# Kernel tuning notes

Measured on AMD Instinct MI355X. Metric: run time of the kernel, lower is better.

## Reference

```python
import jax, jax.numpy as jnp
import numpy as np

EPS = 1e-12  # torch F.normalize default eps


def setup_inputs() -> dict:
    key = jax.random.key(0)
    k1, k2, k3 = jax.random.split(key, 3)
    B, T, S = 128, 512, 256
    emission_trajectory = jax.random.uniform(k1, (B, T, S), dtype=jnp.float32)
    weight = jax.random.normal(k2, (S, S), dtype=jnp.float32)
    initial_state = jax.random.normal(k3, (S,), dtype=jnp.float32)
    return {
        "emission_trajectory": emission_trajectory,
        "weight": weight,
        "initial_state": initial_state,
    }


def reference(emission_trajectory, weight, initial_state):
    B, T, S = emission_trajectory.shape
    # row-stochastic transition matrix (softmax over dim=1)
    transition = jax.nn.softmax(weight, axis=1)  # [S, S]
    # initial belief (training path: softmax of learned logits), broadcast to batch
    next_state0 = jnp.broadcast_to(jax.nn.softmax(initial_state), (B, S))

    emissions_t = jnp.swapaxes(emission_trajectory, 0, 1)  # [T, B, S]

    def step(next_state, emission_k):
        # Bayes update: elementwise likelihood, L1 normalize (torch p=1 normalize)
        unnorm = next_state * emission_k  # [B, S]
        l1 = jnp.sum(jnp.abs(unnorm), axis=1, keepdims=True)
        state = unnorm / jnp.maximum(l1, EPS)
        # predict: small GEMM [B,S] @ [S,S]
        next_state = state @ transition
        return next_state, next_state

    _, traj = jax.lax.scan(step, next_state0, emissions_t)  # traj: [T, B, S]
    return jnp.swapaxes(traj, 0, 1)  # [B, T, S]
```

## Files before the change

kernel.cpp:

```cpp
#include <hip/hip_runtime.h>
#include <stdint.h>

namespace {

constexpr int Tn = 512;
constexpr int Sn = 256;
constexpr float EPS = 1e-12f;

typedef _Float16 f16x8 __attribute__((ext_vector_type(8)));
typedef float    f32x4 __attribute__((ext_vector_type(4)));

__device__ __forceinline__ void wg_barrier_lds() {
    asm volatile("s_waitcnt lgkmcnt(0)" ::: "memory");
    __builtin_amdgcn_s_barrier();
}

__launch_bounds__(256, 1)
__global__ void hmm_kernel(const float* __restrict__ emission,
                           const float* __restrict__ weight,
                           const float* __restrict__ init,
                           float* __restrict__ out)
{
    const int tid  = threadIdx.x;
    const int wv   = tid >> 6;
    const int lane = tid & 63;
    const int g    = lane >> 4;
    const int jj   = lane & 15;
    const int b    = blockIdx.x;

    __shared__ __align__(16) _Float16 wf16[2][Sn];
    __shared__ __align__(16) float    s_m[Sn];
    __shared__ __align__(16) float    s_z[Sn];

    {
        const float* wr = weight + (size_t)tid * Sn;
        float m = -3.402823466e38f;
        #pragma unroll 4
        for (int i = 0; i < Sn; i += 4) {
            float4 v = *reinterpret_cast<const float4*>(wr + i);
            m = fmaxf(m, fmaxf(fmaxf(v.x, v.y), fmaxf(v.z, v.w)));
        }
        float z0 = 0.f, z1 = 0.f, z2 = 0.f, z3 = 0.f;
        #pragma unroll 4
        for (int i = 0; i < Sn; i += 4) {
            float4 v = *reinterpret_cast<const float4*>(wr + i);
            z0 += expf(v.x - m); z1 += expf(v.y - m);
            z2 += expf(v.z - m); z3 += expf(v.w - m);
        }
        s_m[tid] = m;
        s_z[tid] = 1.f / ((z0 + z1) + (z2 + z3));
        __syncthreads();
    }

    f16x8 bf[4][8];
    #pragma unroll
    for (int s = 0; s < 4; ++s) {
        const int col = 64 * wv + 16 * s + jj;
        #pragma unroll
        for (int ck = 0; ck < 8; ++ck) {
            #pragma unroll
            for (int i = 0; i < 8; ++i) {
                const int k = ck * 32 + g * 8 + i;
                bf[s][ck][i] =
                    (_Float16)(expf(weight[(size_t)k * Sn + col] - s_m[k]) * s_z[k]);
            }
        }
    }
    const f16x8 ones8 = {(_Float16)1.f, (_Float16)1.f, (_Float16)1.f, (_Float16)1.f,
                         (_Float16)1.f, (_Float16)1.f, (_Float16)1.f, (_Float16)1.f};

    const float* em = emission + (size_t)b * Tn * Sn + tid;
    float*       op = out      + (size_t)b * Tn * Sn + tid;
    {
        float i0 = init[lane], i1 = init[lane + 64],
              i2 = init[lane + 128], i3 = init[lane + 192];
        float mx = fmaxf(fmaxf(i0, i1), fmaxf(i2, i3));
        #pragma unroll
        for (int o = 32; o >= 1; o >>= 1) mx = fmaxf(mx, __shfl_xor(mx, o));
        float zz = expf(i0 - mx) + expf(i1 - mx) + expf(i2 - mx) + expf(i3 - mx);
        #pragma unroll
        for (int o = 32; o >= 1; o >>= 1) zz += __shfl_xor(zz, o);
        float u  = expf(init[tid] - mx) / zz;
        float w0 = u * em[0];
        wf16[0][tid] = (_Float16)w0;
    }
    float enext = em[Sn];
    __syncthreads();

#define MFMA(A, B, D) __builtin_amdgcn_mfma_f32_16x16x32_f16((A), (B), (D), 0, 0, 0)

    #pragma unroll 1
    for (int t = 0; t < Tn; ++t) {
        const int p = t & 1;

        f16x8 af[8];
        #pragma unroll
        for (int ck = 0; ck < 8; ++ck)
            af[ck] = *reinterpret_cast<const f16x8*>(&wf16[p][ck * 32 + g * 8]);

        __builtin_amdgcn_sched_barrier(0);

        f32x4 d0 = {0.f,0.f,0.f,0.f}, d1 = {0.f,0.f,0.f,0.f};
        f32x4 d2 = {0.f,0.f,0.f,0.f}, d3 = {0.f,0.f,0.f,0.f};
        f32x4 dS = {0.f,0.f,0.f,0.f};
        #pragma unroll
        for (int ck = 0; ck < 8; ++ck) {
            d0 = MFMA(af[ck], bf[0][ck], d0);
            d1 = MFMA(af[ck], bf[1][ck], d1);
            d2 = MFMA(af[ck], bf[2][ck], d2);
            d3 = MFMA(af[ck], bf[3][ck], d3);
            dS = MFMA(af[ck], ones8, dS);
        }

        float y  = (g == 0) ? d0[0] : (g == 1) ? d1[0] : (g == 2) ? d2[0] : d3[0];
        float l1 = fmaxf(dS[0], EPS);

        uint32_t ebits = __float_as_uint(l1) & 0x7f800000u;
        float sigma = __uint_as_float(0x7f000000u - ebits);

        float wn = (y * sigma) * enext;
        wf16[p ^ 1][tid] = (_Float16)wn;

        op[(size_t)t * Sn] = y * (1.f / l1);

        const int tp = (t + 2 < Tn) ? (t + 2) : (Tn - 1);
        enext = em[(size_t)tp * Sn];

        wg_barrier_lds();
    }

#undef MFMA
}

}

extern "C" void kernel_launch(void* const* d_in, const int* in_sizes, int n_in,
                              void* d_out, int out_size, void* d_ws, size_t ws_size,
                              hipStream_t stream) {
    const float* emission = (const float*)d_in[0];
    const float* weight   = (const float*)d_in[1];
    const float* init     = (const float*)d_in[2];
    float* outp = (float*)d_out;
    const int Bn = in_sizes[0] / (Tn * Sn);

    hipLaunchKernelGGL(hmm_kernel, dim3(Bn), dim3(256), 0, stream,
                       emission, weight, init, outp);
}
```

Before: 279.7 us.

## Process two batch rows per workgroup sharing transition fragments

Each workgroup now runs the recurrence for two batch rows at once. It reuses the register-resident transition fragments and interleaves independent MFMA chains for the two rows inside each time step. The aim is to hide MFMA and LDS latency on the serial per-step dependency chain and to amortize the setup softmax. In exchange, the grid shrinks to half as many workgroups, so fewer compute units are used and per-step work doubles.

```diff
diff --git a/kernel.cpp b/kernel.cpp
--- a/kernel.cpp
+++ b/kernel.cpp
@@ -19,16 +19,19 @@
 __global__ void hmm_kernel(const float* __restrict__ emission,
                            const float* __restrict__ weight,
                            const float* __restrict__ init,
-                           float* __restrict__ out)
+                           float* __restrict__ out,
+                           int Bn)
 {
     const int tid  = threadIdx.x;
     const int wv   = tid >> 6;
     const int lane = tid & 63;
     const int g    = lane >> 4;
     const int jj   = lane & 15;
-    const int b    = blockIdx.x;
+    const int rA   = blockIdx.x * 2;
+    const int rB   = (rA + 1 < Bn) ? rA + 1 : rA;
 
-    __shared__ __align__(16) _Float16 wf16[2][Sn];
+    __shared__ __align__(16) _Float16 wfA[2][Sn];
+    __shared__ __align__(16) _Float16 wfB[2][Sn];
     __shared__ __align__(16) float    s_m[Sn];
     __shared__ __align__(16) float    s_z[Sn];
 
@@ -69,8 +72,10 @@
     const f16x8 ones8 = {(_Float16)1.f, (_Float16)1.f, (_Float16)1.f, (_Float16)1.f,
                          (_Float16)1.f, (_Float16)1.f, (_Float16)1.f, (_Float16)1.f};
 
-    const float* em = emission + (size_t)b * Tn * Sn + tid;
-    float*       op = out      + (size_t)b * Tn * Sn + tid;
+    const float* emA = emission + (size_t)rA * Tn * Sn + tid;
+    const float* emB = emission + (size_t)rB * Tn * Sn + tid;
+    float*       opA = out      + (size_t)rA * Tn * Sn + tid;
+    float*       opB = out      + (size_t)rB * Tn * Sn + tid;
     {
         float i0 = init[lane], i1 = init[lane + 64],
               i2 = init[lane + 128], i3 = init[lane + 192];
@@ -80,11 +85,12 @@
         float zz = expf(i0 - mx) + expf(i1 - mx) + expf(i2 - mx) + expf(i3 - mx);
         #pragma unroll
         for (int o = 32; o >= 1; o >>= 1) zz += __shfl_xor(zz, o);
-        float u  = expf(init[tid] - mx) / zz;
-        float w0 = u * em[0];
-        wf16[0][tid] = (_Float16)w0;
+        float u = expf(init[tid] - mx) / zz;
+        wfA[0][tid] = (_Float16)(u * emA[0]);
+        wfB[0][tid] = (_Float16)(u * emB[0]);
     }
-    float enext = em[Sn];
+    float enextA = emA[Sn];
+    float enextB = emB[Sn];
     __syncthreads();
 
 #define MFMA(A, B, D) __builtin_amdgcn_mfma_f32_16x16x32_f16((A), (B), (D), 0, 0, 0)
@@ -93,38 +99,47 @@
     for (int t = 0; t < Tn; ++t) {
         const int p = t & 1;
 
-        f16x8 af[8];
+        f16x8 afA[8], afB[8];
         #pragma unroll
-        for (int ck = 0; ck < 8; ++ck)
-            af[ck] = *reinterpret_cast<const f16x8*>(&wf16[p][ck * 32 + g * 8]);
-
+        for (int ck = 0; ck < 8; ++ck) {
+            afA[ck] = *reinterpret_cast<const f16x8*>(&wfA[p][ck * 32 + g * 8]);
+            afB[ck] = *reinterpret_cast<const f16x8*>(&wfB[p][ck * 32 + g * 8]);
+        }
         __builtin_amdgcn_sched_barrier(0);
 
-        f32x4 d0 = {0.f,0.f,0.f,0.f}, d1 = {0.f,0.f,0.f,0.f};
-        f32x4 d2 = {0.f,0.f,0.f,0.f}, d3 = {0.f,0.f,0.f,0.f};
-        f32x4 dS = {0.f,0.f,0.f,0.f};
+        f32x4 a0 = {0,0,0,0}, a1 = {0,0,0,0}, a2 = {0,0,0,0}, a3 = {0,0,0,0};
+        f32x4 b0 = {0,0,0,0}, b1 = {0,0,0,0}, b2 = {0,0,0,0}, b3 = {0,0,0,0};
+        f32x4 aS = {0,0,0,0}, bS = {0,0,0,0};
         #pragma unroll
         for (int ck = 0; ck < 8; ++ck) {
-            d0 = MFMA(af[ck], bf[0][ck], d0);
-            d1 = MFMA(af[ck], bf[1][ck], d1);
-            d2 = MFMA(af[ck], bf[2][ck], d2);
-            d3 = MFMA(af[ck], bf[3][ck], d3);
-            dS = MFMA(af[ck], ones8, dS);
+            a0 = MFMA(afA[ck], bf[0][ck], a0);  b0 = MFMA(afB[ck], bf[0][ck], b0);
+            a1 = MFMA(afA[ck], bf[1][ck], a1);  b1 = MFMA(afB[ck], bf[1][ck], b1);
+            a2 = MFMA(afA[ck], bf[2][ck], a2);  b2 = MFMA(afB[ck], bf[2][ck], b2);
+            a3 = MFMA(afA[ck], bf[3][ck], a3);  b3 = MFMA(afB[ck], bf[3][ck], b3);
+            aS = MFMA(afA[ck], ones8,    aS);   bS = MFMA(afB[ck], ones8,    bS);
         }
 
-        float y  = (g == 0) ? d0[0] : (g == 1) ? d1[0] : (g == 2) ? d2[0] : d3[0];
-        float l1 = fmaxf(dS[0], EPS);
+        float yA  = (g == 0) ? a0[0] : (g == 1) ? a1[0] : (g == 2) ? a2[0] : a3[0];
+        float yB  = (g == 0) ? b0[0] : (g == 1) ? b1[0] : (g == 2) ? b2[0] : b3[0];
+        float l1A = fmaxf(aS[0], EPS);
+        float l1B = fmaxf(bS[0], EPS);
 
-        uint32_t ebits = __float_as_uint(l1) & 0x7f800000u;
-        float sigma = __uint_as_float(0x7f000000u - ebits);
+        float sigmaA = __uint_as_float(0x7f000000u -
+                        (__float_as_uint(l1A) & 0x7f800000u));
+        float sigmaB = __uint_as_float(0x7f000000u -
+                        (__float_as_uint(l1B) & 0x7f800000u));
 
-        float wn = (y * sigma) * enext;
-        wf16[p ^ 1][tid] = (_Float16)wn;
+        float wnA = (yA * sigmaA) * enextA;
+        float wnB = (yB * sigmaB) * enextB;
+        wfA[p ^ 1][tid] = (_Float16)wnA;
+        wfB[p ^ 1][tid] = (_Float16)wnB;
 
-        op[(size_t)t * Sn] = y * (1.f / l1);
+        opA[(size_t)t * Sn] = yA * (1.f / l1A);
+        opB[(size_t)t * Sn] = yB * (1.f / l1B);
 
         const int tp = (t + 2 < Tn) ? (t + 2) : (Tn - 1);
-        enext = em[(size_t)tp * Sn];
+        enextA = emA[(size_t)tp * Sn];
+        enextB = emB[(size_t)tp * Sn];
 
         wg_barrier_lds();
     }
@@ -142,7 +157,8 @@
     const float* init     = (const float*)d_in[2];
     float* outp = (float*)d_out;
     const int Bn = in_sizes[0] / (Tn * Sn);
+    const int nblk = (Bn + 1) / 2;
 
-    hipLaunchKernelGGL(hmm_kernel, dim3(Bn), dim3(256), 0, stream,
-                       emission, weight, init, outp);
+    hipLaunchKernelGGL(hmm_kernel, dim3(nblk), dim3(256), 0, stream,
+                       emission, weight, init, outp, Bn);
 }
```

Measured after the change: 504.0 us. 80.2% more time.

## Halve workgroup to two waves, each computing 128 output columns

Applied to the files above, without the earlier changes.

Reduces the block from four waves to two, with each wave holding twice as many transition-matrix fragments in registers and issuing eight MFMA tiles per step instead of four. Each thread now handles two state columns for emission loads, LDS writes and output stores. This cuts barrier participants and the redundant row-sum MFMA, but doubles the serial MFMA chain per wave and raises register pressure.

```diff
diff --git a/kernel.cpp b/kernel.cpp
--- a/kernel.cpp
+++ b/kernel.cpp
@@ -15,7 +15,7 @@
     __builtin_amdgcn_s_barrier();
 }
 
-__launch_bounds__(256, 1)
+__launch_bounds__(128, 1)
 __global__ void hmm_kernel(const float* __restrict__ emission,
                            const float* __restrict__ weight,
                            const float* __restrict__ init,
@@ -28,12 +28,17 @@
     const int jj   = lane & 15;
     const int b    = blockIdx.x;
 
+    const int c1 = 128 * wv + 16 * g + jj;
+    const int c2 = c1 + 64;
+
     __shared__ __align__(16) _Float16 wf16[2][Sn];
     __shared__ __align__(16) float    s_m[Sn];
     __shared__ __align__(16) float    s_z[Sn];
 
-    {
-        const float* wr = weight + (size_t)tid * Sn;
+    #pragma unroll
+    for (int h = 0; h < 2; ++h) {
+        const int row = tid + 128 * h;
+        const float* wr = weight + (size_t)row * Sn;
         float m = -3.402823466e38f;
         #pragma unroll 4
         for (int i = 0; i < Sn; i += 4) {
@@ -47,15 +52,15 @@
             z0 += expf(v.x - m); z1 += expf(v.y - m);
             z2 += expf(v.z - m); z3 += expf(v.w - m);
         }
-        s_m[tid] = m;
-        s_z[tid] = 1.f / ((z0 + z1) + (z2 + z3));
-        __syncthreads();
+        s_m[row] = m;
+        s_z[row] = 1.f / ((z0 + z1) + (z2 + z3));
     }
+    __syncthreads();
 
-    f16x8 bf[4][8];
+    f16x8 bf[8][8];
     #pragma unroll
-    for (int s = 0; s < 4; ++s) {
-        const int col = 64 * wv + 16 * s + jj;
+    for (int s = 0; s < 8; ++s) {
+        const int col = 128 * wv + 16 * s + jj;
         #pragma unroll
         for (int ck = 0; ck < 8; ++ck) {
             #pragma unroll
@@ -69,8 +74,10 @@
     const f16x8 ones8 = {(_Float16)1.f, (_Float16)1.f, (_Float16)1.f, (_Float16)1.f,
                          (_Float16)1.f, (_Float16)1.f, (_Float16)1.f, (_Float16)1.f};
 
-    const float* em = emission + (size_t)b * Tn * Sn + tid;
-    float*       op = out      + (size_t)b * Tn * Sn + tid;
+    const float* em1 = emission + (size_t)b * Tn * Sn + c1;
+    const float* em2 = emission + (size_t)b * Tn * Sn + c2;
+    float*       op1 = out      + (size_t)b * Tn * Sn + c1;
+    float*       op2 = out      + (size_t)b * Tn * Sn + c2;
     {
         float i0 = init[lane], i1 = init[lane + 64],
               i2 = init[lane + 128], i3 = init[lane + 192];
@@ -80,11 +87,13 @@
         float zz = expf(i0 - mx) + expf(i1 - mx) + expf(i2 - mx) + expf(i3 - mx);
         #pragma unroll
         for (int o = 32; o >= 1; o >>= 1) zz += __shfl_xor(zz, o);
-        float u  = expf(init[tid] - mx) / zz;
-        float w0 = u * em[0];
-        wf16[0][tid] = (_Float16)w0;
+        float u1 = expf(init[c1] - mx) / zz;
+        float u2 = expf(init[c2] - mx) / zz;
+        wf16[0][c1] = (_Float16)(u1 * em1[0]);
+        wf16[0][c2] = (_Float16)(u2 * em2[0]);
     }
-    float enext = em[Sn];
+    float enext1 = em1[Sn];
+    float enext2 = em2[Sn];
     __syncthreads();
 
 #define MFMA(A, B, D) __builtin_amdgcn_mfma_f32_16x16x32_f16((A), (B), (D), 0, 0, 0)
@@ -97,34 +106,43 @@
         #pragma unroll
         for (int ck = 0; ck < 8; ++ck)
             af[ck] = *reinterpret_cast<const f16x8*>(&wf16[p][ck * 32 + g * 8]);
-
         __builtin_amdgcn_sched_barrier(0);
 
-        f32x4 d0 = {0.f,0.f,0.f,0.f}, d1 = {0.f,0.f,0.f,0.f};
-        f32x4 d2 = {0.f,0.f,0.f,0.f}, d3 = {0.f,0.f,0.f,0.f};
-        f32x4 dS = {0.f,0.f,0.f,0.f};
+        f32x4 d0 = {0,0,0,0}, d1 = {0,0,0,0}, d2 = {0,0,0,0}, d3 = {0,0,0,0};
+        f32x4 d4 = {0,0,0,0}, d5 = {0,0,0,0}, d6 = {0,0,0,0}, d7 = {0,0,0,0};
+        f32x4 dS = {0,0,0,0};
         #pragma unroll
         for (int ck = 0; ck < 8; ++ck) {
             d0 = MFMA(af[ck], bf[0][ck], d0);
             d1 = MFMA(af[ck], bf[1][ck], d1);
             d2 = MFMA(af[ck], bf[2][ck], d2);
             d3 = MFMA(af[ck], bf[3][ck], d3);
-            dS = MFMA(af[ck], ones8, dS);
+            d4 = MFMA(af[ck], bf[4][ck], d4);
+            d5 = MFMA(af[ck], bf[5][ck], d5);
+            d6 = MFMA(af[ck], bf[6][ck], d6);
+            d7 = MFMA(af[ck], bf[7][ck], d7);
+            dS = MFMA(af[ck], ones8,    dS);
         }
 
-        float y  = (g == 0) ? d0[0] : (g == 1) ? d1[0] : (g == 2) ? d2[0] : d3[0];
+        float y1 = (g == 0) ? d0[0] : (g == 1) ? d1[0] : (g == 2) ? d2[0] : d3[0];
+        float y2 = (g == 0) ? d4[0] : (g == 1) ? d5[0] : (g == 2) ? d6[0] : d7[0];
         float l1 = fmaxf(dS[0], EPS);
 
-        uint32_t ebits = __float_as_uint(l1) & 0x7f800000u;
-        float sigma = __uint_as_float(0x7f000000u - ebits);
+        float sigma = __uint_as_float(0x7f000000u -
+                        (__float_as_uint(l1) & 0x7f800000u));
 
-        float wn = (y * sigma) * enext;
-        wf16[p ^ 1][tid] = (_Float16)wn;
+        float wn1 = (y1 * sigma) * enext1;
+        float wn2 = (y2 * sigma) * enext2;
+        wf16[p ^ 1][c1] = (_Float16)wn1;
+        wf16[p ^ 1][c2] = (_Float16)wn2;
 
-        op[(size_t)t * Sn] = y * (1.f / l1);
+        float inv = 1.f / l1;
+        op1[(size_t)t * Sn] = y1 * inv;
+        op2[(size_t)t * Sn] = y2 * inv;
 
         const int tp = (t + 2 < Tn) ? (t + 2) : (Tn - 1);
-        enext = em[(size_t)tp * Sn];
+        enext1 = em1[(size_t)tp * Sn];
+        enext2 = em2[(size_t)tp * Sn];
 
         wg_barrier_lds();
     }
@@ -143,6 +161,6 @@
     float* outp = (float*)d_out;
     const int Bn = in_sizes[0] / (Tn * Sn);
 
-    hipLaunchKernelGGL(hmm_kernel, dim3(Bn), dim3(256), 0, stream,
+    hipLaunchKernelGGL(hmm_kernel, dim3(Bn), dim3(128), 0, stream,
                        emission, weight, init, outp);
 }
```

Result: slower. 546.9 us (+95.5%).
